# Kernel tuning notes

Measured on AMD Instinct MI355X. Metric: run time of the kernel, lower is better.

Reference implementation:

```python
import jax, jax.numpy as jnp
import numpy as np

N = 4096      # batch_size
D = 256       # projection dim
TEMP = 0.5    # temperature


def setup_inputs() -> dict:
    key = jax.random.key(0)
    k1, k2 = jax.random.split(key)
    return {
        "emb_i": jax.random.normal(k1, (N, D), dtype=jnp.float32),
        "emb_j": jax.random.normal(k2, (N, D), dtype=jnp.float32),
    }


def reference(emb_i, emb_j):
    # L2-normalize rows (F.normalize, dim=1)
    z_i = emb_i / jnp.maximum(jnp.linalg.norm(emb_i, axis=1, keepdims=True), 1e-12)
    z_j = emb_j / jnp.maximum(jnp.linalg.norm(emb_j, axis=1, keepdims=True), 1e-12)
    rep = jnp.concatenate([z_i, z_j], axis=0)            # [2N, D]

    # cosine similarity of unit vectors == dot product -> GEMM instead of O(N^2 D) broadcast
    sim = rep @ rep.T                                    # [2N, 2N]

    # positives: diag(sim, +N) and diag(sim, -N) are both sum(z_i*z_j, axis=1)
    pos_ij = jnp.sum(z_i * z_j, axis=1)                  # [N]
    positives = jnp.concatenate([pos_ij, pos_ij], axis=0)  # [2N]

    # mask keeps exactly the two cross-view blocks (main diagonal lies in same-view blocks)
    idx = jnp.arange(2 * N)
    mask = (idx[:, None] < N) != (idx[None, :] < N)      # [2N, 2N] bool

    nominator = jnp.exp(positives / TEMP)                # [2N]
    denominator = jnp.sum(jnp.where(mask, jnp.exp(sim / TEMP), 0.0), axis=1)  # [2N]

    loss_partial = -jnp.log(nominator / (0.5 * denominator))
    return jnp.sum(loss_partial) / (2 * N)
```

## Files before the change

kernel.cpp:

```cpp
#include <hip/hip_runtime.h>
#include <math.h>

#define NROWS 4096
#define DDIM  256
#define BM 128
#define BN 256
#define BK 64
#define LOG2E2 2.8853900817779268f

typedef __attribute__((ext_vector_type(8))) short short8;
typedef __attribute__((ext_vector_type(4))) float f32x4;

__device__ __forceinline__ unsigned short f2bf(float f) {
    unsigned int u = __float_as_uint(f);
    u += 0x7fffu + ((u >> 16) & 1u);
    return (unsigned short)(u >> 16);
}

__device__ __forceinline__ float exp2_fast(float x) {
#if __has_builtin(__builtin_amdgcn_exp2f)
    return __builtin_amdgcn_exp2f(x);
#else
    return exp2f(x);
#endif
}

#define GLOAD_LDS16(gsrc, ldst)                                          \
    __builtin_amdgcn_global_load_lds(                                    \
        (__attribute__((address_space(1))) void*)(gsrc),                 \
        (__attribute__((address_space(3))) void*)(ldst), 16, 0, 0)

__global__ __launch_bounds__(256) void normalize_kernel(
    const float* __restrict__ emb_i, const float* __restrict__ emb_j,
    unsigned short* __restrict__ zi, unsigned short* __restrict__ zj,
    float* __restrict__ pos, float* __restrict__ sums )
{
    if (threadIdx.x < 8) sums[blockIdx.x * 8 + threadIdx.x] = 0.0f;

    const int wave = threadIdx.x >> 6;
    const int lane = threadIdx.x & 63;
    const int row  = blockIdx.x * 4 + wave;

    const float4 vi = *((const float4*)(emb_i + (size_t)row * DDIM) + lane);
    const float4 vj = *((const float4*)(emb_j + (size_t)row * DDIM) + lane);

    float ssi = vi.x*vi.x + vi.y*vi.y + vi.z*vi.z + vi.w*vi.w;
    float ssj = vj.x*vj.x + vj.y*vj.y + vj.z*vj.z + vj.w*vj.w;
    #pragma unroll
    for (int m = 1; m < 64; m <<= 1) {
        ssi += __shfl_xor(ssi, m);
        ssj += __shfl_xor(ssj, m);
    }
    const float ri = 1.0f / fmaxf(sqrtf(ssi), 1e-12f);
    const float rj = 1.0f / fmaxf(sqrtf(ssj), 1e-12f);

    const float zix = vi.x*ri, ziy = vi.y*ri, ziz = vi.z*ri, ziw = vi.w*ri;
    const float zjx = vj.x*rj, zjy = vj.y*rj, zjz = vj.z*rj, zjw = vj.w*rj;

    float p = zix*zjx + ziy*zjy + ziz*zjz + ziw*zjw;
    #pragma unroll
    for (int m = 1; m < 64; m <<= 1) p += __shfl_xor(p, m);
    if (lane == 0) pos[row] = p;

    ushort4 oi = { f2bf(zix*LOG2E2), f2bf(ziy*LOG2E2), f2bf(ziz*LOG2E2), f2bf(ziw*LOG2E2) };
    ushort4 oj = { f2bf(zjx), f2bf(zjy), f2bf(zjz), f2bf(zjw) };
    *((ushort4*)(zi + (size_t)row * DDIM) + lane) = oi;
    *((ushort4*)(zj + (size_t)row * DDIM) + lane) = oj;
}

__global__ __launch_bounds__(256, 2) void gemm_fused_kernel(
    const unsigned short* __restrict__ zi, const unsigned short* __restrict__ zj,
    float* __restrict__ rowsum, float* __restrict__ colsum)
{
    __shared__ unsigned short As[BM * BK];
    __shared__ unsigned short Bs[BN * BK];

    const int tid  = threadIdx.x;
    const int lane = tid & 63;
    const int wave = tid >> 6;
    const int g    = lane >> 4;
    const int fr   = lane & 15;
    const int wr   = wave >> 1;
    const int wc   = wave & 1;
    const int bm   = blockIdx.x * BM;
    const int bn   = blockIdx.y * BN;

    f32x4 acc[4][8] = {};

    const int srow = tid >> 3;
    const int soff = (((tid & 7) ^ (srow & 7)) << 3);

    for (int k0 = 0; k0 < DDIM; k0 += BK) {
        #pragma unroll
        for (int it = 0; it < 4; ++it) {
            const int row = it * 32 + srow;
            const int lb  = (it * 256 + wave * 64) << 3;
            GLOAD_LDS16(zi + (size_t)(bm + row) * DDIM + k0 + soff, As + lb);
        }
        #pragma unroll
        for (int it = 0; it < 8; ++it) {
            const int row = it * 32 + srow;
            const int lb  = (it * 256 + wave * 64) << 3;
            GLOAD_LDS16(zj + (size_t)(bn + row) * DDIM + k0 + soff, Bs + lb);
        }
        __syncthreads();

        #pragma unroll
        for (int kk = 0; kk < 2; ++kk) {
            const int coff = (((kk * 4 + g) ^ (fr & 7)) << 3);
            short8 a[4], b[8];
            #pragma unroll
            for (int mi = 0; mi < 4; ++mi)
                a[mi] = *(const short8*)&As[(wr * 64 + mi * 16 + fr) * BK + coff];
            #pragma unroll
            for (int ni = 0; ni < 8; ++ni)
                b[ni] = *(const short8*)&Bs[(wc * 128 + ni * 16 + fr) * BK + coff];
            #pragma unroll
            for (int mi = 0; mi < 4; ++mi)
                #pragma unroll
                for (int ni = 0; ni < 8; ++ni)
                    acc[mi][ni] = __builtin_amdgcn_mfma_f32_16x16x32_bf16(
                        a[mi], b[ni], acc[mi][ni], 0, 0, 0);
        }
        __syncthreads();
    }

    float rp[4][4];
    float cp[8] = {0.f,0.f,0.f,0.f,0.f,0.f,0.f,0.f};
    #pragma unroll
    for (int mi = 0; mi < 4; ++mi)
        #pragma unroll
        for (int j = 0; j < 4; ++j) rp[mi][j] = 0.f;

    #pragma unroll
    for (int mi = 0; mi < 4; ++mi)
        #pragma unroll
        for (int ni = 0; ni < 8; ++ni)
            #pragma unroll
            for (int j = 0; j < 4; ++j) {
                const float e = exp2_fast(acc[mi][ni][j]);
                rp[mi][j] += e;
                cp[ni]    += e;
            }

    #pragma unroll
    for (int mi = 0; mi < 4; ++mi)
        #pragma unroll
        for (int j = 0; j < 4; ++j) {
            float v = rp[mi][j];
            v += __shfl_xor(v, 1); v += __shfl_xor(v, 2);
            v += __shfl_xor(v, 4); v += __shfl_xor(v, 8);
            if (fr == 0)
                atomicAdd(&rowsum[bm + wr * 64 + mi * 16 + g * 4 + j], v);
        }

    #pragma unroll
    for (int ni = 0; ni < 8; ++ni) {
        float v = cp[ni];
        v += __shfl_xor(v, 16); v += __shfl_xor(v, 32);
        if (g == 0)
            atomicAdd(&colsum[bn + wc * 128 + ni * 16 + fr], v);
    }
}

__global__ __launch_bounds__(512) void finalize_kernel(
    const float* __restrict__ pos, const float* __restrict__ rowsum,
    const float* __restrict__ colsum, float* __restrict__ out)
{
    float s = 0.0f;
    for (int r = threadIdx.x; r < NROWS; r += 512) {
        s += -4.0f * pos[r] + logf(0.25f * rowsum[r] * colsum[r]);
    }
    __shared__ float part[8];
    #pragma unroll
    for (int m = 1; m < 64; m <<= 1) s += __shfl_xor(s, m);
    if ((threadIdx.x & 63) == 0) part[threadIdx.x >> 6] = s;
    __syncthreads();
    if (threadIdx.x == 0) {
        float t = 0.f;
        #pragma unroll
        for (int w = 0; w < 8; ++w) t += part[w];
        out[0] = t / (2.0f * NROWS);
    }
}

extern "C" void kernel_launch(void* const* d_in, const int* in_sizes, int n_in,
                              void* d_out, int out_size, void* d_ws, size_t ws_size,
                              hipStream_t stream)
{
    const float* emb_i = (const float*)d_in[0];
    const float* emb_j = (const float*)d_in[1];

    unsigned short* zi = (unsigned short*)d_ws;
    unsigned short* zj = zi + (size_t)NROWS * DDIM;
    float* pos    = (float*)(zj + (size_t)NROWS * DDIM);
    float* rowsum = pos + NROWS;
    float* colsum = rowsum + NROWS;

    normalize_kernel<<<NROWS / 4, 256, 0, stream>>>(emb_i, emb_j, zi, zj, pos, rowsum);

    dim3 grid(NROWS / BM, NROWS / BN);
    gemm_fused_kernel<<<grid, 256, 0, stream>>>(zi, zj, rowsum, colsum);

    finalize_kernel<<<1, 512, 0, stream>>>(pos, rowsum, colsum, (float*)d_out);
}
```

Measured before the change: 77.35 us.

## Load MFMA operands directly from global memory, dropping LDS staging

The GEMM kernel stops staging A and B tiles in shared memory through global_load_lds with barriers. Each wave now loads its own short8 fragments straight from global memory for all eight K-steps, with the loop fully unrolled. This removes LDS traffic, the swizzle logic and the __syncthreads calls. In exchange, data shared between the two waves of a block is fetched twice through L1/L2, loads are 16-byte strided by row, and register pressure from the unrolled loads may rise.

```diff
diff --git a/kernel.cpp b/kernel.cpp
--- a/kernel.cpp
+++ b/kernel.cpp
@@ -5,7 +5,6 @@
 #define DDIM  256
 #define BM 128
 #define BN 256
-#define BK 64
 #define LOG2E2 2.8853900817779268f
 
 typedef __attribute__((ext_vector_type(8))) short short8;
@@ -24,11 +23,6 @@
     return exp2f(x);
 #endif
 }
-
-#define GLOAD_LDS16(gsrc, ldst)                                          \
-    __builtin_amdgcn_global_load_lds(                                    \
-        (__attribute__((address_space(1))) void*)(gsrc),                 \
-        (__attribute__((address_space(3))) void*)(ldst), 16, 0, 0)
 
 __global__ __launch_bounds__(256) void normalize_kernel(
     const float* __restrict__ emb_i, const float* __restrict__ emb_j,
@@ -72,9 +66,6 @@
     const unsigned short* __restrict__ zi, const unsigned short* __restrict__ zj,
     float* __restrict__ rowsum, float* __restrict__ colsum)
 {
-    __shared__ unsigned short As[BM * BK];
-    __shared__ unsigned short Bs[BN * BK];
-
     const int tid  = threadIdx.x;
     const int lane = tid & 63;
     const int wave = tid >> 6;
@@ -87,42 +78,24 @@
 
     f32x4 acc[4][8] = {};
 
-    const int srow = tid >> 3;
-    const int soff = (((tid & 7) ^ (srow & 7)) << 3);
+    const unsigned short* pA = zi + (size_t)(bm + wr * 64  + fr) * DDIM + g * 8;
+    const unsigned short* pB = zj + (size_t)(bn + wc * 128 + fr) * DDIM + g * 8;
 
-    for (int k0 = 0; k0 < DDIM; k0 += BK) {
+    #pragma unroll
+    for (int kk = 0; kk < 8; ++kk) {
+        short8 a[4], b[8];
         #pragma unroll
-        for (int it = 0; it < 4; ++it) {
-            const int row = it * 32 + srow;
-            const int lb  = (it * 256 + wave * 64) << 3;
-            GLOAD_LDS16(zi + (size_t)(bm + row) * DDIM + k0 + soff, As + lb);
-        }
+        for (int mi = 0; mi < 4; ++mi)
+            a[mi] = *(const short8*)(pA + (size_t)mi * 16 * DDIM + kk * 32);
         #pragma unroll
-        for (int it = 0; it < 8; ++it) {
-            const int row = it * 32 + srow;
-            const int lb  = (it * 256 + wave * 64) << 3;
-            GLOAD_LDS16(zj + (size_t)(bn + row) * DDIM + k0 + soff, Bs + lb);
-        }
-        __syncthreads();
-
+        for (int ni = 0; ni < 8; ++ni)
+            b[ni] = *(const short8*)(pB + (size_t)ni * 16 * DDIM + kk * 32);
         #pragma unroll
-        for (int kk = 0; kk < 2; ++kk) {
-            const int coff = (((kk * 4 + g) ^ (fr & 7)) << 3);
-            short8 a[4], b[8];
-            #pragma unroll
-            for (int mi = 0; mi < 4; ++mi)
-                a[mi] = *(const short8*)&As[(wr * 64 + mi * 16 + fr) * BK + coff];
+        for (int mi = 0; mi < 4; ++mi)
             #pragma unroll
             for (int ni = 0; ni < 8; ++ni)
-                b[ni] = *(const short8*)&Bs[(wc * 128 + ni * 16 + fr) * BK + coff];
-            #pragma unroll
-            for (int mi = 0; mi < 4; ++mi)
-                #pragma unroll
-                for (int ni = 0; ni < 8; ++ni)
-                    acc[mi][ni] = __builtin_amdgcn_mfma_f32_16x16x32_bf16(
-                        a[mi], b[ni], acc[mi][ni], 0, 0, 0);
-        }
-        __syncthreads();
+                acc[mi][ni] = __builtin_amdgcn_mfma_f32_16x16x32_bf16(
+                    a[mi], b[ni], acc[mi][ni], 0, 0, 0);
     }
 
     float rp[4][4];
```

Result: slower. 93.09 us (+20.4%).

## Switch similarity GEMM from bf16 to fp8 e4m3 MFMA

Applied to the files above, without the earlier changes.

The normalize kernel now writes the normalized embeddings as packed fp8 e4m3 bytes, using the hardware pack-convert builtin when it is available. The GEMM loads half as many bytes into LDS with a new 16-byte-slot swizzle and uses the fp8 16x16x32 MFMA instead of the bf16 one. This cuts global and LDS traffic and uses the higher-throughput fp8 matrix path. The cost is much coarser similarity values feeding exp, which risks loss accuracy.

```diff
diff --git a/kernel.cpp b/kernel.cpp
--- a/kernel.cpp
+++ b/kernel.cpp
@@ -8,14 +8,7 @@
 #define BK 64
 #define LOG2E2 2.8853900817779268f
 
-typedef __attribute__((ext_vector_type(8))) short short8;
 typedef __attribute__((ext_vector_type(4))) float f32x4;
-
-__device__ __forceinline__ unsigned short f2bf(float f) {
-    unsigned int u = __float_as_uint(f);
-    u += 0x7fffu + ((u >> 16) & 1u);
-    return (unsigned short)(u >> 16);
-}
 
 __device__ __forceinline__ float exp2_fast(float x) {
 #if __has_builtin(__builtin_amdgcn_exp2f)
@@ -25,6 +18,35 @@
 #endif
 }
 
+__device__ __forceinline__ unsigned char f2e4m3(float f) {
+    unsigned int u = __float_as_uint(f);
+    unsigned int s = (u >> 24) & 0x80;
+    float a = fabsf(f);
+    if (a >= 448.0f) return (unsigned char)(s | 0x7E);
+    if (a < 0.0009765625f) return (unsigned char)s;
+    int exp = (int)((u >> 23) & 0xFF) - 127;
+    if (exp < -6) {
+        int t = (int)(a * 512.0f + 0.5f);
+        return (unsigned char)(s | (unsigned char)t);
+    }
+    unsigned int r = u + 0x0007FFFF + ((u >> 20) & 1);
+    exp = (int)((r >> 23) & 0xFF) - 127;
+    if (exp > 8) return (unsigned char)(s | 0x7E);
+    unsigned int mant = (r >> 20) & 7;
+    return (unsigned char)(s | (unsigned int)((exp + 7) << 3) | mant);
+}
+
+__device__ __forceinline__ unsigned int pack4_e4m3(float a, float b, float c, float d) {
+#if __has_builtin(__builtin_amdgcn_cvt_pk_fp8_f32)
+    int v = __builtin_amdgcn_cvt_pk_fp8_f32(a, b, 0, 0);
+    v = __builtin_amdgcn_cvt_pk_fp8_f32(c, d, v, 1);
+    return (unsigned int)v;
+#else
+    return (unsigned int)f2e4m3(a) | ((unsigned int)f2e4m3(b) << 8) |
+           ((unsigned int)f2e4m3(c) << 16) | ((unsigned int)f2e4m3(d) << 24);
+#endif
+}
+
 #define GLOAD_LDS16(gsrc, ldst)                                          \
     __builtin_amdgcn_global_load_lds(                                    \
         (__attribute__((address_space(1))) void*)(gsrc),                 \
@@ -32,7 +54,7 @@
 
 __global__ __launch_bounds__(256) void normalize_kernel(
     const float* __restrict__ emb_i, const float* __restrict__ emb_j,
-    unsigned short* __restrict__ zi, unsigned short* __restrict__ zj,
+    unsigned char* __restrict__ zi, unsigned char* __restrict__ zj,
     float* __restrict__ pos, float* __restrict__ sums )
 {
     if (threadIdx.x < 8) sums[blockIdx.x * 8 + threadIdx.x] = 0.0f;
@@ -62,18 +84,18 @@
     for (int m = 1; m < 64; m <<= 1) p += __shfl_xor(p, m);
     if (lane == 0) pos[row] = p;
 
-    ushort4 oi = { f2bf(zix*LOG2E2), f2bf(ziy*LOG2E2), f2bf(ziz*LOG2E2), f2bf(ziw*LOG2E2) };
-    ushort4 oj = { f2bf(zjx), f2bf(zjy), f2bf(zjz), f2bf(zjw) };
-    *((ushort4*)(zi + (size_t)row * DDIM) + lane) = oi;
-    *((ushort4*)(zj + (size_t)row * DDIM) + lane) = oj;
+    *(unsigned int*)(zi + (size_t)row * DDIM + lane * 4) =
+        pack4_e4m3(zix*LOG2E2, ziy*LOG2E2, ziz*LOG2E2, ziw*LOG2E2);
+    *(unsigned int*)(zj + (size_t)row * DDIM + lane * 4) =
+        pack4_e4m3(zjx, zjy, zjz, zjw);
 }
 
 __global__ __launch_bounds__(256, 2) void gemm_fused_kernel(
-    const unsigned short* __restrict__ zi, const unsigned short* __restrict__ zj,
+    const unsigned char* __restrict__ zi, const unsigned char* __restrict__ zj,
     float* __restrict__ rowsum, float* __restrict__ colsum)
 {
-    __shared__ unsigned short As[BM * BK];
-    __shared__ unsigned short Bs[BN * BK];
+    __shared__ unsigned char As[BM * BK];
+    __shared__ unsigned char Bs[BN * BK];
 
     const int tid  = threadIdx.x;
     const int lane = tid & 63;
@@ -87,39 +109,41 @@
 
     f32x4 acc[4][8] = {};
 
-    const int srow = tid >> 3;
-    const int soff = (((tid & 7) ^ (srow & 7)) << 3);
-
     for (int k0 = 0; k0 < DDIM; k0 += BK) {
         #pragma unroll
+        for (int it = 0; it < 2; ++it) {
+            const int L   = it * 256 + tid;
+            const int row = L >> 2;
+            const int sl  = (L & 3) ^ (row & 3);
+            GLOAD_LDS16(zi + (size_t)(bm + row) * DDIM + k0 + sl * 16,
+                        &As[(it * 256 + wave * 64) * 16]);
+        }
+        #pragma unroll
         for (int it = 0; it < 4; ++it) {
-            const int row = it * 32 + srow;
-            const int lb  = (it * 256 + wave * 64) << 3;
-            GLOAD_LDS16(zi + (size_t)(bm + row) * DDIM + k0 + soff, As + lb);
-        }
-        #pragma unroll
-        for (int it = 0; it < 8; ++it) {
-            const int row = it * 32 + srow;
-            const int lb  = (it * 256 + wave * 64) << 3;
-            GLOAD_LDS16(zj + (size_t)(bn + row) * DDIM + k0 + soff, Bs + lb);
+            const int L   = it * 256 + tid;
+            const int row = L >> 2;
+            const int sl  = (L & 3) ^ (row & 3);
+            GLOAD_LDS16(zj + (size_t)(bn + row) * DDIM + k0 + sl * 16,
+                        &Bs[(it * 256 + wave * 64) * 16]);
         }
         __syncthreads();
 
         #pragma unroll
         for (int kk = 0; kk < 2; ++kk) {
-            const int coff = (((kk * 4 + g) ^ (fr & 7)) << 3);
-            short8 a[4], b[8];
+            const int slot = kk * 2 + (g >> 1);
+            const int boff = ((slot ^ (fr & 3)) << 4) + ((g & 1) << 3);
+            long long a[4], b[8];
             #pragma unroll
             for (int mi = 0; mi < 4; ++mi)
-                a[mi] = *(const short8*)&As[(wr * 64 + mi * 16 + fr) * BK + coff];
+                a[mi] = *(const long long*)&As[(wr * 64 + mi * 16 + fr) * BK + boff];
             #pragma unroll
             for (int ni = 0; ni < 8; ++ni)
-                b[ni] = *(const short8*)&Bs[(wc * 128 + ni * 16 + fr) * BK + coff];
+                b[ni] = *(const long long*)&Bs[(wc * 128 + ni * 16 + fr) * BK + boff];
             #pragma unroll
             for (int mi = 0; mi < 4; ++mi)
                 #pragma unroll
                 for (int ni = 0; ni < 8; ++ni)
-                    acc[mi][ni] = __builtin_amdgcn_mfma_f32_16x16x32_bf16(
+                    acc[mi][ni] = __builtin_amdgcn_mfma_f32_16x16x32_fp8_fp8(
                         a[mi], b[ni], acc[mi][ni], 0, 0, 0);
         }
         __syncthreads();
@@ -191,8 +215,8 @@
     const float* emb_i = (const float*)d_in[0];
     const float* emb_j = (const float*)d_in[1];
 
-    unsigned short* zi = (unsigned short*)d_ws;
-    unsigned short* zj = zi + (size_t)NROWS * DDIM;
+    unsigned char* zi = (unsigned char*)d_ws;
+    unsigned char* zj = zi + (size_t)NROWS * DDIM;
     float* pos    = (float*)(zj + (size_t)NROWS * DDIM);
     float* rowsum = pos + NROWS;
     float* colsum = rowsum + NROWS;
```

Measured after the change: 77.70 us. About the same (+0.5%).
